# Kernel optimization log

Hardware: AMD Instinct MI355X
Metric: run time of the kernel (lower is better)

## Reference

```python
import math
import jax, jax.numpy as jnp
import numpy as np

D_MODEL, STATE_DIM, SEQ_L = 256, 64, 8192


def setup_inputs() -> dict:
    key = jax.random.key(0)
    ks = jax.random.split(key, 6)
    d, N = D_MODEL, STATE_DIM
    s = 1.0 / math.sqrt(N)
    return {
        "Lambda_re": jax.random.normal(ks[0], (d, N), jnp.float32),
        "Lambda_im": jax.random.normal(ks[1], (d, N), jnp.float32),
        "P_re": jax.random.normal(ks[2], (d, N), jnp.float32) * s,
        "P_im": jax.random.normal(ks[3], (d, N), jnp.float32) * s,
        "B_re": jax.random.normal(ks[4], (d, N), jnp.float32) * s,
        "B_im": jnp.zeros((d, N), jnp.float32),
        "log_dt": jax.random.uniform(ks[5], (d,), jnp.float32,
                                     math.log(1e-3), math.log(0.1)),
        "D": jnp.zeros((d,), jnpp := jnp.float32) if False else jnp.zeros((d,), jnp.float32),
        "L": SEQ_L,
    }


def reference(Lambda_re, Lambda_im, P_re, P_im, B_re, B_im, log_dt, D, L):
    # NPLR / Cauchy-Woodbury S4 kernel (learn_cd=False -> C = B, D is a zero buffer)
    Lam = (-jax.nn.softplus(Lambda_re) + 1j * Lambda_im).astype(jnp.complex64)  # [d, N]
    P = (P_re + 1j * P_im).astype(jnp.complex64)                                # [d, N]
    B = (B_re + 1j * B_im).astype(jnp.complex64)                                # [d, N]
    dt = jnp.exp(log_dt)                                                        # [d]

    k = jnp.arange(L)
    z = jnp.exp((-2j * jnp.pi / L) * k).astype(jnp.complex64)                   # [L] roots of unity
    eps = jnp.finfo(jnp.float32).eps
    denom_z = 1.0 + z
    denom_z = jnp.where(jnp.abs(denom_z) < eps, jnp.complex64(eps), denom_z)

    # Bilinear-transform frequencies g: [d, L] complex
    g = (2.0 / dt)[:, None] * ((1.0 - z) / denom_z)[None, :]

    # Cauchy resolvent R: [d, L, N] complex (the dominant intermediate)
    R = 1.0 / (g[:, :, None] - Lam[:, None, :])

    Pc, Bc = jnp.conj(P), jnp.conj(B)
    PRB = jnp.einsum('dn,dln,dn->dl', Pc, R, B)
    PRP = jnp.einsum('dn,dln,dn->dl', Pc, R, P)
    BRB = jnp.einsum('dn,dln,dn->dl', Bc, R, B)
    BRP = jnp.einsum('dn,dln,dn->dl', Bc, R, P)

    # Woodbury rank-1 correction, then undo the bilinear prefactor
    K_hat = (2.0 / denom_z)[None, :] * (BRB - BRP * PRB / (1.0 + PRP))          # [d, L]
    K = jnp.fft.ifft(K_hat, n=L, axis=-1).real.astype(jnp.float32)
    return (K, D)
```

## Files before the change

### kernel.cpp

```cpp
#include <hip/hip_runtime.h>
#include <math.h>

#ifndef M_PI
#define M_PI 3.14159265358979323846
#endif

#define DMODEL 256
#define NSTATE 64
#define LSEQ   8192
#define INVL   (1.0f/8192.0f)

#define OFF_TW  0
#define OFF_DN  (6144*8)
#define OFF_CDT (OFF_DN + DMODEL*NSTATE*48)
#define OFF_KT  (OFF_CDT + 1024)

__device__ __forceinline__ float sin_rev(float r) {
#if __has_builtin(__builtin_amdgcn_sinf)
  return __builtin_amdgcn_sinf(r);
#else
  return __sinf(r * 6.283185307179586f);
#endif
}
__device__ __forceinline__ float cos_rev(float r) {
#if __has_builtin(__builtin_amdgcn_cosf)
  return __builtin_amdgcn_cosf(r);
#else
  return __cosf(r * 6.283185307179586f);
#endif
}

__device__ __forceinline__ float2 cmul(float2 a, float2 b) {
  return make_float2(a.x*b.x - a.y*b.y, a.x*b.y + a.y*b.x);
}

__device__ __forceinline__ float2 woodbury(float2 S1, float2 S2, float2 S3,
                                           float2 S4, float T) {
  float nr = (S1.x*S1.x - S1.y*S1.y) + (S2.x*S2.x - S2.y*S2.y);
  float ni = 2.0f*(S1.x*S1.y + S2.x*S2.y);
  float dr = 1.0f + S3.x, di = S3.y;
  float inv = __builtin_amdgcn_rcpf(fmaf(dr, dr, di*di));
  float qr = (nr*dr + ni*di) * inv;
  float qi = (ni*dr - nr*di) * inv;
  float vr = S4.x - qr, vi = S4.y - qi;
  return make_float2((vr - T*vi)*INVL, (vi + T*vr)*INVL);
}

__global__ __launch_bounds__(256) void precompute_kernel(
    const float* __restrict__ Lre, const float* __restrict__ Lim,
    const float* __restrict__ Pre, const float* __restrict__ Pim,
    const float* __restrict__ Bre, const float* __restrict__ Bim,
    const float* __restrict__ log_dt, char* __restrict__ ws)
{
  const int t = blockIdx.x * blockDim.x + threadIdx.x;
  float2* tw  = (float2*)(ws + OFF_TW);
  float4* dn  = (float4*)(ws + OFF_DN);
  float*  cdt = (float*)(ws + OFF_CDT);

  if (t < 6144) {
    double th = (2.0 * M_PI / (double)LSEQ) * (double)t;
    double s, c; sincos(th, &s, &c);
    tw[t] = make_float2((float)c, (float)s);
  }
  {
    float lre = Lre[t], lim = Lim[t];
    float pre = Pre[t], pim = Pim[t];
    float bre = Bre[t], bim = Bim[t];
    float sp = fmaxf(lre, 0.0f) + log1pf(expf(-fabsf(lre)));
    float w1r = pre*bre + pim*bim;
    float w1i = pre*bim - pim*bre;
    float w2  = pre*pre + pim*pim;
    float w3  = bre*bre + bim*bim;
    dn[3*t]   = make_float4(lim, sp*sp, w1r*sp, w1i*sp);
    dn[3*t+1] = make_float4(w2*sp, w3*sp, w1r, w1i);
    dn[3*t+2] = make_float4(w2, w3, 0.0f, 0.0f);
  }
  if (t < DMODEL) cdt[t] = 2.0f * expf(-log_dt[t]);
}

__global__ __launch_bounds__(256, 8) void cauchy_kernel(
    const float4* __restrict__ dn_all, const float* __restrict__ cdt,
    float4* __restrict__ kt)
{
  const int d = blockIdx.y;
  const int b = blockIdx.x * 256 + threadIdx.x;
  const float4* dn = dn_all + (size_t)d * (3*NSTATE);
  const float c = cdt[d];

  const unsigned p = (unsigned)(2*b);
  const unsigned r = __brev(p) >> 19;
  const int kA = (int)(((r & 0x0555u) << 1) | ((r & 0x0AAAu) >> 1));
  const float rev = (float)kA * (1.0f/16384.0f);
  const float sA = sin_rev(rev), cA = cos_rev(rev);
  float TA = sA * __builtin_amdgcn_rcpf(cA);
  float TB = -cA * __builtin_amdgcn_rcpf(sA);
  TA = fminf(fmaxf(TA, -1e7f), 1e7f);
  TB = fminf(fmaxf(TB, -1e7f), 1e7f);
  const float gA = c * TA, gB = c * TB;

  float2 S1a = {0,0}, S2a = {0,0}, S3a = {0,0}, S4a = {0,0};
  float2 S1b = {0,0}, S2b = {0,0}, S3b = {0,0}, S4b = {0,0};
#pragma unroll 4
  for (int n = 0; n < NSTATE; ++n) {
    const float4 q0 = dn[3*n];
    const float4 q1 = dn[3*n+1];
    const float4 q2 = dn[3*n+2];
    {
      const float dim = gA - q0.x;
      const float inv = __builtin_amdgcn_rcpf(fmaf(dim, dim, q0.y));
      const float dI  = dim * inv;
      S1a.x = fmaf(q0.z, inv, S1a.x);  S1a.y = fmaf(q1.z, -dI, S1a.y);
      S2a.x = fmaf(q0.w, inv, S2a.x);  S2a.y = fmaf(q1.w, -dI, S2a.y);
      S3a.x = fmaf(q1.x, inv, S3a.x);  S3a.y = fmaf(q2.x, -dI, S3a.y);
      S4a.x = fmaf(q1.y, inv, S4a.x);  S4a.y = fmaf(q2.y, -dI, S4a.y);
    }
    {
      const float dim = gB - q0.x;
      const float inv = __builtin_amdgcn_rcpf(fmaf(dim, dim, q0.y));
      const float dI  = dim * inv;
      S1b.x = fmaf(q0.z, inv, S1b.x);  S1b.y = fmaf(q1.z, -dI, S1b.y);
      S2b.x = fmaf(q0.w, inv, S2b.x);  S2b.y = fmaf(q1.w, -dI, S2b.y);
      S3b.x = fmaf(q1.x, inv, S3b.x);  S3b.y = fmaf(q2.x, -dI, S3b.y);
      S4b.x = fmaf(q1.y, inv, S4b.x);  S4b.y = fmaf(q2.y, -dI, S4b.y);
    }
  }
  const float2 KA = woodbury(S1a, S2a, S3a, S4a, TA);
  const float2 KB = woodbury(S1b, S2b, S3b, S4b, TB);
  kt[(size_t)d * 4096 + b] = make_float4(KA.x + KB.x, KA.y + KB.y,
                                         KA.x - KB.x, KA.y - KB.y);
}

__global__ __launch_bounds__(1024) void ifft_kernel(
    const float4* __restrict__ kt, const float2* __restrict__ tw,
    const float* __restrict__ Din, float* __restrict__ out)
{
  __shared__ __align__(16) float2 xy[LSEQ];
  const int d = blockIdx.x;
  const int t = threadIdx.x;
  const float4* row = kt + (size_t)d * 4096;

  for (int i = t; i < 4096; i += 1024) ((float4*)xy)[i] = row[i];
  __syncthreads();

#pragma unroll
  for (int s = 0; s < 6; ++s) {
    const int h = 2 << (2*s);
    const int twsh = 10 - 2*s;
#pragma unroll
    for (int j = 0; j < 2; ++j) {
      const int bb = t + (j << 10);
      const int pos = bb & (h - 1);
      const int i0 = ((bb >> (1 + 2*s)) << (3 + 2*s)) + pos;
      const int ti = pos << twsh;
      const float2 w1 = tw[ti];
      const float2 w2 = tw[2*ti];
      const float2 w3 = tw[3*ti];
      const float2 x0 = xy[i0];
      const float2 x1 = xy[i0 + h];
      const float2 x2 = xy[i0 + 2*h];
      const float2 x3 = xy[i0 + 3*h];
      const float2 t1 = cmul(w1, x1);
      const float2 t2 = cmul(w2, x2);
      const float2 t3 = cmul(w3, x3);
      const float2 u0 = make_float2(x0.x + t2.x, x0.y + t2.y);
      const float2 u1 = make_float2(x0.x - t2.x, x0.y - t2.y);
      const float2 u2 = make_float2(t1.x + t3.x, t1.y + t3.y);
      const float2 vv = make_float2(t1.x - t3.x, t1.y - t3.y);
      xy[i0]         = make_float2(u0.x + u2.x, u0.y + u2.y);
      xy[i0 + h]     = make_float2(u1.x - vv.y, u1.y + vv.x);
      xy[i0 + 2*h]   = make_float2(u0.x - u2.x, u0.y - u2.y);
      xy[i0 + 3*h]   = make_float2(u1.x + vv.y, u1.y - vv.x);
    }
    __syncthreads();
  }

  float* orow = out + (size_t)d * LSEQ;
  for (int i = t; i < LSEQ; i += 1024) orow[i] = xy[i].x;

  if (d == 0 && t < DMODEL) out[(size_t)DMODEL * LSEQ + t] = Din[t];
}

extern "C" void kernel_launch(void* const* d_in, const int* in_sizes, int n_in,
                              void* d_out, int out_size, void* d_ws, size_t ws_size,
                              hipStream_t stream)
{
  const float* Lre    = (const float*)d_in[0];
  const float* Lim    = (const float*)d_in[1];
  const float* Pre    = (const float*)d_in[2];
  const float* Pim    = (const float*)d_in[3];
  const float* Bre    = (const float*)d_in[4];
  const float* Bim    = (const float*)d_in[5];
  const float* log_dt = (const float*)d_in[6];
  const float* Din    = (const float*)d_in[7];
  float* out = (float*)d_out;
  char* ws = (char*)d_ws;

  hipLaunchKernelGGL(precompute_kernel, dim3(64), dim3(256), 0, stream,
                     Lre, Lim, Pre, Pim, Bre, Bim, log_dt, ws);
  hipLaunchKernelGGL(cauchy_kernel, dim3(16, DMODEL), dim3(256), 0, stream,
                     (const float4*)(ws + OFF_DN), (const float*)(ws + OFF_CDT),
                     (float4*)(ws + OFF_KT));
  hipLaunchKernelGGL(ifft_kernel, dim3(DMODEL), dim3(1024), 0, stream,
                     (const float4*)(ws + OFF_KT), (const float2*)(ws + OFF_TW),
                     Din, out);
}
```

Before: 129.9 us.

## Process four frequency points per Cauchy thread and swizzle IFFT shared memory

Each Cauchy thread now evaluates two bit-reversed frequency pairs (four points) per loaded state vector, which halves the grid and amortizes the per-state loads over more arithmetic. The launch-bounds occupancy hint drops from 8 to 4 to leave room for the extra accumulators. Separately, IFFT shared-memory indexing gets an XOR swizzle to reduce LDS bank conflicts in the radix-4 butterflies. Costs are higher register pressure, fewer waves in flight for Cauchy, and extra index arithmetic in the FFT.

```diff
diff --git a/kernel.cpp b/kernel.cpp
--- a/kernel.cpp
+++ b/kernel.cpp
@@ -33,6 +33,8 @@
 __device__ __forceinline__ float2 cmul(float2 a, float2 b) {
   return make_float2(a.x*b.x - a.y*b.y, a.x*b.y + a.y*b.x);
 }
+
+__device__ __forceinline__ int swz(int i) { return i ^ ((i >> 3) & 0xE); }
 
 __device__ __forceinline__ float2 woodbury(float2 S1, float2 S2, float2 S3,
                                            float2 S4, float T) {
@@ -78,7 +80,7 @@
   if (t < DMODEL) cdt[t] = 2.0f * expf(-log_dt[t]);
 }
 
-__global__ __launch_bounds__(256, 8) void cauchy_kernel(
+__global__ __launch_bounds__(256, 4) void cauchy_kernel(
     const float4* __restrict__ dn_all, const float* __restrict__ cdt,
     float4* __restrict__ kt)
 {
@@ -87,47 +89,58 @@
   const float4* dn = dn_all + (size_t)d * (3*NSTATE);
   const float c = cdt[d];
 
-  const unsigned p = (unsigned)(2*b);
-  const unsigned r = __brev(p) >> 19;
-  const int kA = (int)(((r & 0x0555u) << 1) | ((r & 0x0AAAu) >> 1));
-  const float rev = (float)kA * (1.0f/16384.0f);
-  const float sA = sin_rev(rev), cA = cos_rev(rev);
-  float TA = sA * __builtin_amdgcn_rcpf(cA);
-  float TB = -cA * __builtin_amdgcn_rcpf(sA);
-  TA = fminf(fmaxf(TA, -1e7f), 1e7f);
-  TB = fminf(fmaxf(TB, -1e7f), 1e7f);
-  const float gA = c * TA, gB = c * TB;
-
-  float2 S1a = {0,0}, S2a = {0,0}, S3a = {0,0}, S4a = {0,0};
-  float2 S1b = {0,0}, S2b = {0,0}, S3b = {0,0}, S4b = {0,0};
-#pragma unroll 4
+  const unsigned r = __brev((unsigned)(2*b)) >> 19;
+  const int kA0 = (int)(((r & 0x0555u) << 1) | ((r & 0x0AAAu) >> 1));
+  const int kA1 = kA0 + 2;
+  const float rev0 = (float)kA0 * (1.0f/16384.0f);
+  const float rev1 = (float)kA1 * (1.0f/16384.0f);
+  const float s0 = sin_rev(rev0), c0 = cos_rev(rev0);
+  const float s1 = sin_rev(rev1), c1 = cos_rev(rev1);
+  float TA0 =  s0 * __builtin_amdgcn_rcpf(c0);
+  float TB0 = -c0 * __builtin_amdgcn_rcpf(s0);
+  float TA1 =  s1 * __builtin_amdgcn_rcpf(c1);
+  float TB1 = -c1 * __builtin_amdgcn_rcpf(s1);
+  TA0 = fminf(fmaxf(TA0, -1e7f), 1e7f);
+  TB0 = fminf(fmaxf(TB0, -1e7f), 1e7f);
+  TA1 = fminf(fmaxf(TA1, -1e7f), 1e7f);
+  TB1 = fminf(fmaxf(TB1, -1e7f), 1e7f);
+  const float gA0 = c*TA0, gB0 = c*TB0, gA1 = c*TA1, gB1 = c*TB1;
+
+  float2 S1a0={0,0}, S2a0={0,0}, S3a0={0,0}, S4a0={0,0};
+  float2 S1b0={0,0}, S2b0={0,0}, S3b0={0,0}, S4b0={0,0};
+  float2 S1a1={0,0}, S2a1={0,0}, S3a1={0,0}, S4a1={0,0};
+  float2 S1b1={0,0}, S2b1={0,0}, S3b1={0,0}, S4b1={0,0};
+
+#pragma unroll 2
   for (int n = 0; n < NSTATE; ++n) {
     const float4 q0 = dn[3*n];
     const float4 q1 = dn[3*n+1];
     const float4 q2 = dn[3*n+2];
-    {
-      const float dim = gA - q0.x;
-      const float inv = __builtin_amdgcn_rcpf(fmaf(dim, dim, q0.y));
-      const float dI  = dim * inv;
-      S1a.x = fmaf(q0.z, inv, S1a.x);  S1a.y = fmaf(q1.z, -dI, S1a.y);
-      S2a.x = fmaf(q0.w, inv, S2a.x);  S2a.y = fmaf(q1.w, -dI, S2a.y);
-      S3a.x = fmaf(q1.x, inv, S3a.x);  S3a.y = fmaf(q2.x, -dI, S3a.y);
-      S4a.x = fmaf(q1.y, inv, S4a.x);  S4a.y = fmaf(q2.y, -dI, S4a.y);
+#define CPOINT(G, S1, S2, S3, S4)                                          \
+    {                                                                      \
+      const float dim = (G) - q0.x;                                        \
+      const float inv = __builtin_amdgcn_rcpf(fmaf(dim, dim, q0.y));       \
+      const float dI  = dim * inv;                                         \
+      S1.x = fmaf(q0.z, inv, S1.x);  S1.y = fmaf(q1.z, -dI, S1.y);         \
+      S2.x = fmaf(q0.w, inv, S2.x);  S2.y = fmaf(q1.w, -dI, S2.y);         \
+      S3.x = fmaf(q1.x, inv, S3.x);  S3.y = fmaf(q2.x, -dI, S3.y);         \
+      S4.x = fmaf(q1.y, inv, S4.x);  S4.y = fmaf(q2.y, -dI, S4.y);         \
     }
-    {
-      const float dim = gB - q0.x;
-      const float inv = __builtin_amdgcn_rcpf(fmaf(dim, dim, q0.y));
-      const float dI  = dim * inv;
-      S1b.x = fmaf(q0.z, inv, S1b.x);  S1b.y = fmaf(q1.z, -dI, S1b.y);
-      S2b.x = fmaf(q0.w, inv, S2b.x);  S2b.y = fmaf(q1.w, -dI, S2b.y);
-      S3b.x = fmaf(q1.x, inv, S3b.x);  S3b.y = fmaf(q2.x, -dI, S3b.y);
-      S4b.x = fmaf(q1.y, inv, S4b.x);  S4b.y = fmaf(q2.y, -dI, S4b.y);
-    }
-  }
-  const float2 KA = woodbury(S1a, S2a, S3a, S4a, TA);
-  const float2 KB = woodbury(S1b, S2b, S3b, S4b, TB);
-  kt[(size_t)d * 4096 + b] = make_float4(KA.x + KB.x, KA.y + KB.y,
-                                         KA.x - KB.x, KA.y - KB.y);
+    CPOINT(gA0, S1a0, S2a0, S3a0, S4a0)
+    CPOINT(gB0, S1b0, S2b0, S3b0, S4b0)
+    CPOINT(gA1, S1a1, S2a1, S3a1, S4a1)
+    CPOINT(gB1, S1b1, S2b1, S3b1, S4b1)
+#undef CPOINT
+  }
+  const float2 KA0 = woodbury(S1a0, S2a0, S3a0, S4a0, TA0);
+  const float2 KB0 = woodbury(S1b0, S2b0, S3b0, S4b0, TB0);
+  const float2 KA1 = woodbury(S1a1, S2a1, S3a1, S4a1, TA1);
+  const float2 KB1 = woodbury(S1b1, S2b1, S3b1, S4b1, TB1);
+  float4* orow = kt + (size_t)d * 4096;
+  orow[b]        = make_float4(KA0.x + KB0.x, KA0.y + KB0.y,
+                               KA0.x - KB0.x, KA0.y - KB0.y);
+  orow[b + 2048] = make_float4(KA1.x + KB1.x, KA1.y + KB1.y,
+                               KA1.x - KB1.x, KA1.y - KB1.y);
 }
 
 __global__ __launch_bounds__(1024) void ifft_kernel(
@@ -139,7 +152,10 @@
   const int t = threadIdx.x;
   const float4* row = kt + (size_t)d * 4096;
 
-  for (int i = t; i < 4096; i += 1024) ((float4*)xy)[i] = row[i];
+  for (int i = t; i < 4096; i += 1024) {
+    const float4 v = row[i];
+    *(float4*)&xy[swz(2*i)] = v;
+  }
   __syncthreads();
 
 #pragma unroll
@@ -151,14 +167,18 @@
       const int bb = t + (j << 10);
       const int pos = bb & (h - 1);
       const int i0 = ((bb >> (1 + 2*s)) << (3 + 2*s)) + pos;
+      const int a0 = swz(i0);
+      const int a1 = swz(i0 + h);
+      const int a2 = swz(i0 + 2*h);
+      const int a3 = swz(i0 + 3*h);
       const int ti = pos << twsh;
       const float2 w1 = tw[ti];
       const float2 w2 = tw[2*ti];
       const float2 w3 = tw[3*ti];
-      const float2 x0 = xy[i0];
-      const float2 x1 = xy[i0 + h];
-      const float2 x2 = xy[i0 + 2*h];
-      const float2 x3 = xy[i0 + 3*h];
+      const float2 x0 = xy[a0];
+      const float2 x1 = xy[a1];
+      const float2 x2 = xy[a2];
+      const float2 x3 = xy[a3];
       const float2 t1 = cmul(w1, x1);
       const float2 t2 = cmul(w2, x2);
       const float2 t3 = cmul(w3, x3);
@@ -166,16 +186,16 @@
       const float2 u1 = make_float2(x0.x - t2.x, x0.y - t2.y);
       const float2 u2 = make_float2(t1.x + t3.x, t1.y + t3.y);
       const float2 vv = make_float2(t1.x - t3.x, t1.y - t3.y);
-      xy[i0]         = make_float2(u0.x + u2.x, u0.y + u2.y);
-      xy[i0 + h]     = make_float2(u1.x - vv.y, u1.y + vv.x);
-      xy[i0 + 2*h]   = make_float2(u0.x - u2.x, u0.y - u2.y);
-      xy[i0 + 3*h]   = make_float2(u1.x + vv.y, u1.y - vv.x);
+      xy[a0] = make_float2(u0.x + u2.x, u0.y + u2.y);
+      xy[a1] = make_float2(u1.x - vv.y, u1.y + vv.x);
+      xy[a2] = make_float2(u0.x - u2.x, u0.y - u2.y);
+      xy[a3] = make_float2(u1.x + vv.y, u1.y - vv.x);
     }
     __syncthreads();
   }
 
   float* orow = out + (size_t)d * LSEQ;
-  for (int i = t; i < LSEQ; i += 1024) orow[i] = xy[i].x;
+  for (int i = t; i < LSEQ; i += 1024) orow[i] = xy[swz(i)].x;
 
   if (d == 0 && t < DMODEL) out[(size_t)DMODEL * LSEQ + t] = Din[t];
 }
@@ -197,7 +217,7 @@
 
   hipLaunchKernelGGL(precompute_kernel, dim3(64), dim3(256), 0, stream,
                      Lre, Lim, Pre, Pim, Bre, Bim, log_dt, ws);
-  hipLaunchKernelGGL(cauchy_kernel, dim3(16, DMODEL), dim3(256), 0, stream,
+  hipLaunchKernelGGL(cauchy_kernel, dim3(8, DMODEL), dim3(256), 0, stream,
                      (const float4*)(ws + OFF_DN), (const float*)(ws + OFF_CDT),
                      (float4*)(ws + OFF_KT));
   hipLaunchKernelGGL(ifft_kernel, dim3(DMODEL), dim3(1024), 0, stream,
```

Result: slower. 139.0 us (+7.0%).
